# Optimization experiments

Measured on AMD Instinct MI355X. Metric: run time of the kernel, lower is better.

## Reference

```python
import jax, jax.numpy as jnp
import numpy as np

B, S, D_MODEL, D_ATT = 4, 4096, 512, 64
EPS = 1e-5


def setup_inputs() -> dict:
    key = jax.random.key(0)
    ks = jax.random.split(key, 10)
    s_in = 1.0 / np.sqrt(D_MODEL)
    return {
        "x": jax.random.normal(ks[0], (B, S, D_MODEL), jnp.float32),
        "Wq": jax.random.uniform(ks[1], (D_MODEL, D_ATT), jnp.float32, -s_in, s_in),
        "bq": jax.random.uniform(ks[2], (D_ATT,), jnp.float32, -s_in, s_in),
        "Wk": jax.random.uniform(ks[3], (D_MODEL, D_ATT), jnp.float32, -s_in, s_in),
        "bk": jax.random.uniform(ks[4], (D_ATT,), jnp.float32, -s_in, s_in),
        "Wv": jax.random.uniform(ks[5], (D_MODEL, D_MODEL), jnp.float32, -s_in, s_in),
        "bv": jax.random.uniform(ks[6], (D_MODEL,), jnp.float32, -s_in, s_in),
        "gamma": jnp.ones((D_MODEL,), jnp.float32),
        "beta": jnp.zeros((D_MODEL,), jnp.float32),
    }


def reference(x, Wq, bq, Wk, bk, Wv, bv, gamma, beta):
    # Linear projections (torch Linear: x @ W^T + b; here W stored as [in, out])
    q = jnp.einsum("bsd,de->bse", x, Wq) + bq          # [B,S,d_att]
    k = jnp.einsum("bsd,de->bse", x, Wk) + bk          # [B,S,d_att]
    v = jnp.einsum("bsd,de->bse", x, Wv) + bv          # [B,S,d_model]
    # NOTE: original has NO 1/sqrt(d) scaling -- faithful to source.
    scores = jnp.einsum("bqe,bke->bqk", q, k)          # [B,S,S]
    seq = x.shape[1]
    causal = jnp.tril(jnp.ones((seq, seq), dtype=bool))
    scores = jnp.where(causal, scores, -jnp.inf)
    attn = jax.nn.softmax(scores, axis=-1)
    o = jnp.einsum("bqk,bkd->bqd", attn, v)            # [B,S,d_model]
    # residual + LayerNorm over last dim
    y = x + o
    mu = jnp.mean(y, axis=-1, keepdims=True)
    var = jnp.mean(jnp.square(y - mu), axis=-1, keepdims=True)
    return (y - mu) * jax.lax.rsqrt(var + EPS) * gamma + beta
```

## Files before the change

### kernel.cpp

```cpp
#include <hip/hip_runtime.h>

#define NB 4
#define SEQ 4096
#define DM 512
#define DA 64
#define LOG2E 1.44269504f

typedef __attribute__((ext_vector_type(8))) short bf16x8;
typedef __attribute__((ext_vector_type(4))) float f32x4;
typedef __attribute__((ext_vector_type(16))) float f32x16;
typedef __attribute__((address_space(3))) unsigned int lds_u32;
typedef const __attribute__((address_space(1))) unsigned int glb_u32;

__device__ __forceinline__ unsigned short f2bf(float f) {
  unsigned u = __float_as_uint(f);
  u += 0x7fffu + ((u >> 16) & 1u);
  return (unsigned short)(u >> 16);
}

__device__ __forceinline__ float bf2f(unsigned short h) {
  return __uint_as_float(((unsigned)h) << 16);
}

__device__ __forceinline__ unsigned cvt_pk_bf16(float lo, float hi) {
  unsigned r;
  asm("v_cvt_pk_bf16_f32 %0, %1, %2" : "=v"(r) : "v"(lo), "v"(hi));
  return r;
}

__device__ __forceinline__ float fexp2(float x) {
  float r;
  asm("v_exp_f32 %0, %1" : "=v"(r) : "v"(x));
  return r;
}

__device__ __forceinline__ void g2lds16(const unsigned short* g, unsigned short* l) {
  __builtin_amdgcn_global_load_lds((glb_u32*)g, (lds_u32*)l, 16, 0, 0);
}

__global__ void prep_kernel(const float* __restrict__ x, unsigned short* __restrict__ xb,
                            const float* __restrict__ Wq, const float* __restrict__ bq,
                            const float* __restrict__ Wk, const float* __restrict__ bk,
                            const float* __restrict__ Wv, const float* __restrict__ bv,
                            unsigned short* __restrict__ Wt, float* __restrict__ bias) {
  int bid = blockIdx.x;
  if (bid < 8192) {
    size_t i = ((size_t)bid * blockDim.x + threadIdx.x) * 4;
    float4 v = *(const float4*)(x + i);
    ushort4 o;
    o.x = f2bf(v.x); o.y = f2bf(v.y); o.z = f2bf(v.z); o.w = f2bf(v.w);
    *(ushort4*)(xb + i) = o;
  } else {
    int n = bid - 8192;
    for (int k = threadIdx.x; k < DM; k += blockDim.x) {
      float w;
      if (n < 64)       w = Wq[(size_t)k * DA + n];
      else if (n < 128) w = Wk[(size_t)k * DA + (n - 64)];
      else              w = Wv[(size_t)k * DM + (n - 128)];
      Wt[(size_t)n * DM + k] = f2bf(w);
    }
    if (threadIdx.x == 0)
      bias[n] = (n < 64) ? bq[n] : (n < 128) ? bk[n - 64] : bv[n - 128];
  }
}

__launch_bounds__(256)
__global__ void proj_kernel(const unsigned short* __restrict__ xb,
                            const unsigned short* __restrict__ Wt,
                            const float* __restrict__ bias,
                            unsigned short* __restrict__ qws,
                            unsigned short* __restrict__ kp,
                            unsigned short* __restrict__ vp) {
  int C0 = blockIdx.x * 128;
  int R0 = blockIdx.y * 128;
  int tid = threadIdx.x;
  int w = tid >> 6, lane = tid & 63;
  int g = (lane >> 4) & 3, c15 = lane & 15;
  int wr = w >> 1, wc = w & 1;

  __shared__ unsigned short Ab[2][8192];
  __shared__ unsigned short Bb[2][8192];

  int row0 = tid >> 3;
  int scol = (tid & 7) ^ (row0 & 7);
  const unsigned short* srcA = xb + (size_t)(R0 + row0) * DM + scol * 8;
  const unsigned short* srcB = Wt + (size_t)(C0 + row0) * DM + scol * 8;

  auto stage = [&](int t, int kk) {
    for (int r = 0; r < 4; r++)
      g2lds16(srcA + (size_t)(r * 32) * DM + kk, &Ab[t][(r * 32 + w * 8) * 64]);
    for (int r = 0; r < 4; r++)
      g2lds16(srcB + (size_t)(r * 32) * DM + kk, &Bb[t][(r * 32 + w * 8) * 64]);
  };

  f32x4 acc[4][4];
#pragma unroll
  for (int i = 0; i < 4; i++)
#pragma unroll
    for (int j = 0; j < 4; j++) acc[i][j] = (f32x4)0.0f;

  stage(0, 0);
  __syncthreads();
  int t = 0;
  for (int s = 0; s < 8; s++) {
    if (s < 7) stage(t ^ 1, (s + 1) * 64);
    const unsigned short* A = &Ab[t][0];
    const unsigned short* B = &Bb[t][0];
#pragma unroll
    for (int kc = 0; kc < 2; kc++) {
      bf16x8 a[4], bb2[4];
#pragma unroll
      for (int i = 0; i < 4; i++) {
        int row = wr * 64 + i * 16 + c15;
        a[i] = *(const bf16x8*)&A[row * 64 + (((kc << 2) | g) ^ (row & 7)) * 8];
      }
#pragma unroll
      for (int j = 0; j < 4; j++) {
        int row = wc * 64 + j * 16 + c15;
        bb2[j] = *(const bf16x8*)&B[row * 64 + (((kc << 2) | g) ^ (row & 7)) * 8];
      }
#pragma unroll
      for (int i = 0; i < 4; i++)
#pragma unroll
        for (int j = 0; j < 4; j++)
          acc[i][j] = __builtin_amdgcn_mfma_f32_16x16x32_bf16(a[i], bb2[j], acc[i][j], 0, 0, 0);
    }
    __syncthreads();
    t ^= 1;
  }

  unsigned short* tw = (w < 2) ? (&Ab[0][0] + w * 4608) : (&Bb[0][0] + (w - 2) * 4608);
  int n0 = C0 + wc * 64;
#pragma unroll
  for (int j = 0; j < 4; j++) {
    int ncol = n0 + j * 16 + c15;
    float bv_ = bias[ncol];
    float qs = (ncol < 64) ? LOG2E : 1.0f;
#pragma unroll
    for (int i = 0; i < 4; i++)
#pragma unroll
      for (int r = 0; r < 4; r++) {
        int sl = i * 16 + g * 4 + r;
        tw[sl * 72 + j * 16 + c15] = f2bf((acc[i][j][r] + bv_) * qs);
      }
  }

  int RR = R0 + wr * 64;
  int b = RR >> 12, ktc = (RR & (SEQ - 1)) >> 6;
  if (n0 == 0) {
    for (int it = 0; it < 8; it++) {
      int rid = it * 64 + lane;
      int sl = rid >> 3, grp = rid & 7;
      bf16x8 vd = *(const bf16x8*)&tw[sl * 72 + grp * 8];
      *(bf16x8*)(qws + (size_t)(RR + sl) * DA + grp * 8) = vd;
    }
  } else if (n0 == 64) {
    for (int slot = 0; slot < 8; slot++) {
      bf16x8 vd = *(const bf16x8*)&tw[lane * 72 + slot * 8];
      *(bf16x8*)(kp + ((((size_t)b * 64 + ktc) * 8 + slot) * 64 + lane) * 8) = vd;
    }
  } else {
    int dvbase = n0 - 128;
    int dv = dvbase + lane;
    int dvc2 = dv >> 7, dvrow = dv & 127;
    for (int slot = 0; slot < 8; slot++) {
      union { unsigned short u[8]; bf16x8 h8; } pk;
#pragma unroll
      for (int j = 0; j < 8; j++) {
        int key = ((slot >> 2) << 5) | (((slot >> 1) & 1) << 4) | ((j >> 2) << 3) |
                  ((slot & 1) << 2) | (j & 3);
        pk.u[j] = tw[key * 72 + lane];
      }
      *(bf16x8*)(vp + (((((size_t)(b * 4 + dvc2)) * 64 + ktc) * 8 + slot) * 128 + dvrow) * 8) = pk.h8;
    }
  }
}

__launch_bounds__(256, 3)
__global__ void attn_kernel(const unsigned short* __restrict__ qws,
                            const unsigned short* __restrict__ kp,
                            const unsigned short* __restrict__ vp,
                            unsigned short* __restrict__ ob16) {
  int x = blockIdx.x, b = x >> 2, dvc = x & 3;
  int strip = 127 - blockIdx.y;
  int qrow32 = strip * 32;
  int n = (strip >> 1) + 1;
  int tid = threadIdx.x, w = tid >> 6, lane = tid & 63;
  int l31 = lane & 31, lh = lane >> 5;

  __shared__ unsigned short abuf[4][32][138];
  __shared__ float lbuf[4][32], Lfin[32];

  size_t bS = (size_t)b * SEQ;

  bf16x8 qf[4];
#pragma unroll
  for (int c = 0; c < 4; c++)
    qf[c] = *(const bf16x8*)(qws + (bS + qrow32 + l31) * DA + c * 16 + lh * 8);

  const unsigned short* kbase = kp + (size_t)b * 64 * 4096 + lh * 512 + l31 * 8;
  const unsigned short* vbase = vp + (size_t)(b * 4 + dvc) * 64 * 8192 + lh * 1024 + l31 * 8;

  f32x16 acc[4];
#pragma unroll
  for (int dt = 0; dt < 4; dt++) acc[dt] = (f32x16)0.0f;
  float la0 = 0.0f, la1 = 0.0f, la2 = 0.0f, la3 = 0.0f;

  for (int t = w; t < n; t += 4) {
    const unsigned short* kt_ = kbase + (size_t)t * 4096;
    const unsigned short* vt_ = vbase + (size_t)t * 8192;

    bf16x8 kf[4][2];
#pragma unroll
    for (int c = 0; c < 4; c++)
#pragma unroll
      for (int s2 = 0; s2 < 2; s2++)
        kf[c][s2] = *(const bf16x8*)(kt_ + c * 1024 + s2 * 256);
    bf16x8 vbA[4];
#pragma unroll
    for (int dt = 0; dt < 4; dt++)
      vbA[dt] = *(const bf16x8*)(vt_ + dt * 256);

    f32x16 sc[2];
    sc[0] = (f32x16)0.0f; sc[1] = (f32x16)0.0f;
    __builtin_amdgcn_s_setprio(1);
#pragma unroll
    for (int c = 0; c < 4; c++)
#pragma unroll
      for (int s2 = 0; s2 < 2; s2++)
        sc[s2] = __builtin_amdgcn_mfma_f32_32x32x16_bf16(kf[c][s2], qf[c], sc[s2], 0, 0, 0);
    __builtin_amdgcn_s_setprio(0);

    if (t == n - 1) {
      int kt = t * 64, qrow = qrow32 + l31;
#pragma unroll
      for (int s2 = 0; s2 < 2; s2++)
#pragma unroll
        for (int p = 0; p < 16; p++) {
          int key = kt + s2 * 32 + (p & 3) + 8 * (p >> 2) + 4 * lh;
          if (key > qrow) sc[s2][p] = -1e30f;
        }
    }

#pragma unroll
    for (int s2 = 0; s2 < 2; s2++)
#pragma unroll
      for (int p = 0; p < 16; p += 4) {
        float p0 = fexp2(sc[s2][p + 0]);
        float p1 = fexp2(sc[s2][p + 1]);
        float p2 = fexp2(sc[s2][p + 2]);
        float p3 = fexp2(sc[s2][p + 3]);
        sc[s2][p + 0] = p0; sc[s2][p + 1] = p1;
        sc[s2][p + 2] = p2; sc[s2][p + 3] = p3;
        la0 += p0; la1 += p1; la2 += p2; la3 += p3;
      }

    bf16x8 pa[4];
#pragma unroll
    for (int c = 0; c < 4; c++) {
      union { unsigned u[4]; bf16x8 h; } pu;
      int s2 = c >> 1, o = (c & 1) * 8;
      pu.u[0] = cvt_pk_bf16(sc[s2][o + 0], sc[s2][o + 1]);
      pu.u[1] = cvt_pk_bf16(sc[s2][o + 2], sc[s2][o + 3]);
      pu.u[2] = cvt_pk_bf16(sc[s2][o + 4], sc[s2][o + 5]);
      pu.u[3] = cvt_pk_bf16(sc[s2][o + 6], sc[s2][o + 7]);
      pa[c] = pu.h;
    }

    __builtin_amdgcn_s_setprio(1);
#pragma unroll
    for (int c = 0; c < 4; c++) {
      bf16x8 vbB[4];
      if (c < 3) {
#pragma unroll
        for (int dt = 0; dt < 4; dt++)
          vbB[dt] = *(const bf16x8*)(vt_ + (c + 1) * 2048 + dt * 256);
      }
#pragma unroll
      for (int dt = 0; dt < 4; dt++)
        acc[dt] = __builtin_amdgcn_mfma_f32_32x32x16_bf16(vbA[dt], pa[c], acc[dt], 0, 0, 0);
      if (c < 3) {
#pragma unroll
        for (int dt = 0; dt < 4; dt++) vbA[dt] = vbB[dt];
      }
    }
    __builtin_amdgcn_s_setprio(0);
  }

  float l_run = (la0 + la1) + (la2 + la3);
  l_run += __shfl_xor(l_run, 32);
  if (lh == 0) lbuf[w][l31] = l_run;
  __syncthreads();
  if (w == 0 && lh == 0)
    Lfin[l31] = lbuf[0][l31] + lbuf[1][l31] + lbuf[2][l31] + lbuf[3][l31];
#pragma unroll
  for (int dt = 0; dt < 4; dt++)
#pragma unroll
    for (int p = 0; p < 16; p += 2) {
      int dv = dt * 32 + (p & 3) + 8 * (p >> 2) + 4 * lh;
      *(unsigned*)&abuf[w][l31][dv] = cvt_pk_bf16(acc[dt][p], acc[dt][p + 1]);
    }
  __syncthreads();

  int q = w * 8 + (l31 >> 2);
  int ch = (l31 & 3) * 32 + lh * 16;
  float s[16];
#pragma unroll
  for (int k = 0; k < 16; k++) s[k] = 0.0f;
#pragma unroll
  for (int v = 0; v < 4; v++) {
    bf16x8 a0 = *(const bf16x8*)&abuf[v][q][ch];
    bf16x8 a1 = *(const bf16x8*)&abuf[v][q][ch + 8];
#pragma unroll
    for (int k = 0; k < 8; k++) {
      s[k] += bf2f((unsigned short)a0[k]);
      s[8 + k] += bf2f((unsigned short)a1[k]);
    }
  }
  float inv = 1.0f / Lfin[q];
  union { unsigned u[8]; bf16x8 h[2]; } o;
#pragma unroll
  for (int k = 0; k < 8; k++)
    o.u[k] = cvt_pk_bf16(s[2 * k] * inv, s[2 * k + 1] * inv);
  unsigned short* dst = ob16 + (bS + qrow32 + q) * DM + dvc * 128 + ch;
  *(bf16x8*)dst = o.h[0];
  *(bf16x8*)(dst + 8) = o.h[1];
}

__launch_bounds__(256)
__global__ void ln_kernel(const unsigned short* __restrict__ xb,
                          const unsigned short* __restrict__ o,
                          const float* __restrict__ gamma, const float* __restrict__ beta,
                          float* __restrict__ out) {
  int wid = threadIdx.x >> 6, lane = threadIdx.x & 63;
  size_t row = (size_t)blockIdx.x * 4 + wid;
  size_t base = row * DM + lane * 8;
  bf16x8 xv = *(const bf16x8*)(xb + base);
  bf16x8 ov = *(const bf16x8*)(o + base);
  float y[8];
#pragma unroll
  for (int j = 0; j < 8; j++)
    y[j] = bf2f((unsigned short)xv[j]) + bf2f((unsigned short)ov[j]);
  float s1 = 0.0f, s2 = 0.0f;
  for (int j = 0; j < 8; j++) { s1 += y[j]; s2 += y[j] * y[j]; }
  for (int m = 1; m < 64; m <<= 1) { s1 += __shfl_xor(s1, m); s2 += __shfl_xor(s2, m); }
  float mu = s1 * (1.0f / DM);
  float var = s2 * (1.0f / DM) - mu * mu;
  float rs = rsqrtf(var + 1e-5f);
  int c = lane * 8;
  for (int j = 0; j < 8; j++)
    out[base + j] = (y[j] - mu) * rs * gamma[c + j] + beta[c + j];
}

extern "C" void kernel_launch(void* const* d_in, const int* in_sizes, int n_in,
                              void* d_out, int out_size, void* d_ws, size_t ws_size,
                              hipStream_t stream) {
  const float* x     = (const float*)d_in[0];
  const float* Wq    = (const float*)d_in[1];
  const float* bq    = (const float*)d_in[2];
  const float* Wk    = (const float*)d_in[3];
  const float* bk    = (const float*)d_in[4];
  const float* Wv    = (const float*)d_in[5];
  const float* bv    = (const float*)d_in[6];
  const float* gamma = (const float*)d_in[7];
  const float* beta  = (const float*)d_in[8];
  float* out = (float*)d_out;

  char* ws = (char*)d_ws;
  unsigned short* xb   = (unsigned short*)(ws + 0);
  unsigned short* qws  = (unsigned short*)(ws + 16777216);
  unsigned short* kp   = (unsigned short*)(ws + 18874368);
  unsigned short* vp   = (unsigned short*)(ws + 20971520);
  unsigned short* ob16 = (unsigned short*)(ws + 37748736);
  unsigned short* Wt   = (unsigned short*)(ws + 54525952);
  float*          bias = (float*)(ws + 55181312);

  prep_kernel<<<8832, 256, 0, stream>>>(x, xb, Wq, bq, Wk, bk, Wv, bv, Wt, bias);
  proj_kernel<<<dim3(5, 128), 256, 0, stream>>>(xb, Wt, bias, qws, kp, vp);
  attn_kernel<<<dim3(16, 128), 256, 0, stream>>>(qws, kp, vp, ob16);
  ln_kernel<<<4096, 256, 0, stream>>>(xb, ob16, gamma, beta, out);
}
```

Measured before the change: 132.7 us.

## Shrink LDS in projection and attention kernels to raise occupancy

The projection GEMM drops its LDS double buffer for a single buffer with an extra barrier per k-step, cutting shared memory use. The attention kernel replaces its four-wave LDS reduction buffer with a two-step tree reduction over a half-size buffer and raises launch bounds from 3 to 4 blocks per CU. The aim is higher occupancy, which trades away load/compute overlap in the GEMM, adds barriers, and puts more register pressure on attention.

```diff
diff --git a/kernel.cpp b/kernel.cpp
--- a/kernel.cpp
+++ b/kernel.cpp
@@ -78,19 +78,20 @@
   int g = (lane >> 4) & 3, c15 = lane & 15;
   int wr = w >> 1, wc = w & 1;
 
-  __shared__ unsigned short Ab[2][8192];
-  __shared__ unsigned short Bb[2][8192];
+  __shared__ unsigned short smem[18432];
+  unsigned short* Ab = smem;
+  unsigned short* Bb = smem + 8192;
 
   int row0 = tid >> 3;
   int scol = (tid & 7) ^ (row0 & 7);
   const unsigned short* srcA = xb + (size_t)(R0 + row0) * DM + scol * 8;
   const unsigned short* srcB = Wt + (size_t)(C0 + row0) * DM + scol * 8;
 
-  auto stage = [&](int t, int kk) {
+  auto stage = [&](int kk) {
     for (int r = 0; r < 4; r++)
-      g2lds16(srcA + (size_t)(r * 32) * DM + kk, &Ab[t][(r * 32 + w * 8) * 64]);
+      g2lds16(srcA + (size_t)(r * 32) * DM + kk, &Ab[(r * 32 + w * 8) * 64]);
     for (int r = 0; r < 4; r++)
-      g2lds16(srcB + (size_t)(r * 32) * DM + kk, &Bb[t][(r * 32 + w * 8) * 64]);
+      g2lds16(srcB + (size_t)(r * 32) * DM + kk, &Bb[(r * 32 + w * 8) * 64]);
   };
 
   f32x4 acc[4][4];
@@ -99,25 +100,21 @@
 #pragma unroll
     for (int j = 0; j < 4; j++) acc[i][j] = (f32x4)0.0f;
 
-  stage(0, 0);
-  __syncthreads();
-  int t = 0;
+  stage(0);
   for (int s = 0; s < 8; s++) {
-    if (s < 7) stage(t ^ 1, (s + 1) * 64);
-    const unsigned short* A = &Ab[t][0];
-    const unsigned short* B = &Bb[t][0];
+    __syncthreads();
 #pragma unroll
     for (int kc = 0; kc < 2; kc++) {
       bf16x8 a[4], bb2[4];
 #pragma unroll
       for (int i = 0; i < 4; i++) {
         int row = wr * 64 + i * 16 + c15;
-        a[i] = *(const bf16x8*)&A[row * 64 + (((kc << 2) | g) ^ (row & 7)) * 8];
+        a[i] = *(const bf16x8*)&Ab[row * 64 + (((kc << 2) | g) ^ (row & 7)) * 8];
       }
 #pragma unroll
       for (int j = 0; j < 4; j++) {
         int row = wc * 64 + j * 16 + c15;
-        bb2[j] = *(const bf16x8*)&B[row * 64 + (((kc << 2) | g) ^ (row & 7)) * 8];
+        bb2[j] = *(const bf16x8*)&Bb[row * 64 + (((kc << 2) | g) ^ (row & 7)) * 8];
       }
 #pragma unroll
       for (int i = 0; i < 4; i++)
@@ -125,11 +122,14 @@
         for (int j = 0; j < 4; j++)
           acc[i][j] = __builtin_amdgcn_mfma_f32_16x16x32_bf16(a[i], bb2[j], acc[i][j], 0, 0, 0);
     }
-    __syncthreads();
-    t ^= 1;
-  }
-
-  unsigned short* tw = (w < 2) ? (&Ab[0][0] + w * 4608) : (&Bb[0][0] + (w - 2) * 4608);
+    if (s < 7) {
+      __syncthreads();
+      stage((s + 1) * 64);
+    }
+  }
+  __syncthreads();
+
+  unsigned short* tw = smem + w * 4608;
   int n0 = C0 + wc * 64;
 #pragma unroll
   for (int j = 0; j < 4; j++) {
@@ -176,7 +176,7 @@
   }
 }
 
-__launch_bounds__(256, 3)
+__launch_bounds__(256, 4)
 __global__ void attn_kernel(const unsigned short* __restrict__ qws,
                             const unsigned short* __restrict__ kp,
                             const unsigned short* __restrict__ vp,
@@ -188,8 +188,8 @@
   int tid = threadIdx.x, w = tid >> 6, lane = tid & 63;
   int l31 = lane & 31, lh = lane >> 5;
 
-  __shared__ unsigned short abuf[4][32][138];
-  __shared__ float lbuf[4][32], Lfin[32];
+  __shared__ unsigned short abuf[2][32][138];
+  __shared__ float lbuf[4][32];
 
   size_t bS = (size_t)b * SEQ;
 
@@ -290,41 +290,59 @@
   float l_run = (la0 + la1) + (la2 + la3);
   l_run += __shfl_xor(l_run, 32);
   if (lh == 0) lbuf[w][l31] = l_run;
+
+  if (w >= 2) {
+#pragma unroll
+    for (int dt = 0; dt < 4; dt++)
+#pragma unroll
+      for (int p = 0; p < 16; p += 2) {
+        int dv = dt * 32 + (p & 3) + 8 * (p >> 2) + 4 * lh;
+        *(unsigned*)&abuf[w - 2][l31][dv] = cvt_pk_bf16(acc[dt][p], acc[dt][p + 1]);
+      }
+  }
   __syncthreads();
-  if (w == 0 && lh == 0)
-    Lfin[l31] = lbuf[0][l31] + lbuf[1][l31] + lbuf[2][l31] + lbuf[3][l31];
-#pragma unroll
-  for (int dt = 0; dt < 4; dt++)
-#pragma unroll
-    for (int p = 0; p < 16; p += 2) {
-      int dv = dt * 32 + (p & 3) + 8 * (p >> 2) + 4 * lh;
-      *(unsigned*)&abuf[w][l31][dv] = cvt_pk_bf16(acc[dt][p], acc[dt][p + 1]);
-    }
+  if (w < 2) {
+#pragma unroll
+    for (int dt = 0; dt < 4; dt++)
+#pragma unroll
+      for (int p = 0; p < 16; p += 2) {
+        int dv = dt * 32 + (p & 3) + 8 * (p >> 2) + 4 * lh;
+        unsigned pk = *(const unsigned*)&abuf[w][l31][dv];
+        acc[dt][p]     += bf2f((unsigned short)(pk & 0xffffu));
+        acc[dt][p + 1] += bf2f((unsigned short)(pk >> 16));
+      }
+  }
   __syncthreads();
-
-  int q = w * 8 + (l31 >> 2);
-  int ch = (l31 & 3) * 32 + lh * 16;
-  float s[16];
-#pragma unroll
-  for (int k = 0; k < 16; k++) s[k] = 0.0f;
-#pragma unroll
-  for (int v = 0; v < 4; v++) {
-    bf16x8 a0 = *(const bf16x8*)&abuf[v][q][ch];
-    bf16x8 a1 = *(const bf16x8*)&abuf[v][q][ch + 8];
+  if (w == 1) {
+#pragma unroll
+    for (int dt = 0; dt < 4; dt++)
+#pragma unroll
+      for (int p = 0; p < 16; p += 2) {
+        int dv = dt * 32 + (p & 3) + 8 * (p >> 2) + 4 * lh;
+        *(unsigned*)&abuf[0][l31][dv] = cvt_pk_bf16(acc[dt][p], acc[dt][p + 1]);
+      }
+  }
+  __syncthreads();
+  if (w == 0) {
+    float L = lbuf[0][l31] + lbuf[1][l31] + lbuf[2][l31] + lbuf[3][l31];
+    float inv = 1.0f / L;
+#pragma unroll
+    for (int dt = 0; dt < 4; dt++)
+#pragma unroll
+      for (int p = 0; p < 16; p += 2) {
+        int dv = dt * 32 + (p & 3) + 8 * (p >> 2) + 4 * lh;
+        unsigned pk = *(const unsigned*)&abuf[0][l31][dv];
+        float v0 = (acc[dt][p]     + bf2f((unsigned short)(pk & 0xffffu))) * inv;
+        float v1 = (acc[dt][p + 1] + bf2f((unsigned short)(pk >> 16))) * inv;
+        *(unsigned*)&abuf[1][l31][dv] = cvt_pk_bf16(v0, v1);
+      }
+    int row = lane >> 1, dvh = (lane & 1) * 64;
 #pragma unroll
     for (int k = 0; k < 8; k++) {
-      s[k] += bf2f((unsigned short)a0[k]);
-      s[8 + k] += bf2f((unsigned short)a1[k]);
-    }
-  }
-  float inv = 1.0f / Lfin[q];
-  union { unsigned u[8]; bf16x8 h[2]; } o;
-#pragma unroll
-  for (int k = 0; k < 8; k++)
-    o.u[k] = cvt_pk_bf16(s[2 * k] * inv, s[2 * k + 1] * inv);
-  unsigned short* dst = ob16 + (bS + qrow32 + q) * DM + dvc * 128 + ch;
-  *(bf16x8*)dst = o.h[0];
-  *(bf16x8*)(dst + 8) = o.h[1];
+      bf16x8 o8 = *(const bf16x8*)&abuf[1][row][dvh + k * 8];
+      *(bf16x8*)(ob16 + (bS + qrow32 + row) * DM + dvc * 128 + dvh + k * 8) = o8;
+    }
+  }
 }
 
 __launch_bounds__(256)
```

Result: slower. 243.3 us (+83.4%).
